# Kernel optimization log

Measured on AMD Instinct MI355X. Metric: run time of the kernel, lower is better.

## Reference

```python
import jax, jax.numpy as jnp
import numpy as np

# MLA dims (DeepSeek-V3-lite style)
B, S, DIM = 1, 2048, 2048
H, NOPE, ROPE, VD, LORA = 16, 128, 64, 128, 512
QK_HEAD = NOPE + ROPE  # 192
SCALE = QK_HEAD ** -0.5
EPS = 1e-6


def _rmsnorm(x, w):
    return x * jax.lax.rsqrt(jnp.mean(x * x, axis=-1, keepdims=True) + EPS) * w


def _apply_rope(x, cos, sin):
    # x: [b, s, h, d] with interleaved (real, imag) pairs; cos/sin: [s, d//2]
    x0, x1 = x[..., 0::2], x[..., 1::2]
    c = cos[None, :, None, :]
    s = sin[None, :, None, :]
    y0 = x0 * c - x1 * s
    y1 = x0 * s + x1 * c
    return jnp.stack([y0, y1], axis=-1).reshape(x.shape)


def setup_inputs() -> dict:
    key = jax.random.key(0)
    ks = jax.random.split(key, 6)
    x = jax.random.normal(ks[0], (B, S, DIM), jnp.float32) * 0.02
    wq = jax.random.normal(ks[1], (H * QK_HEAD, DIM), jnp.float32) * 0.02
    wkv_a = jax.random.normal(ks[2], (LORA + ROPE, DIM), jnp.float32) * 0.02
    kv_norm_w = jnp.ones((LORA,), jnp.float32)
    wkv_b = jax.random.normal(ks[3], (H * (NOPE + VD), LORA), jnp.float32) * 0.02
    wo = jax.random.normal(ks[4], (DIM, H * VD), jnp.float32) * 0.02
    # rotary freqs_cis (cos/sin) for qk_rope_head_dim
    inv_freq = 1.0 / (10000.0 ** (np.arange(0, ROPE, 2, dtype=np.float32) / ROPE))
    t = np.arange(S, dtype=np.float32)
    ang = np.outer(t, inv_freq)  # [S, ROPE//2]
    cos = jnp.asarray(np.cos(ang), jnp.float32)
    sin = jnp.asarray(np.sin(ang), jnp.float32)
    return {"x": x, "cos": cos, "sin": sin, "wq": wq, "wkv_a": wkv_a,
            "kv_norm_w": kv_norm_w, "wkv_b": wkv_b, "wo": wo}


def reference(x, cos, sin, wq, wkv_a, kv_norm_w, wkv_b, wo):
    b, s, _ = x.shape
    # queries
    q = (x @ wq.T).reshape(b, s, H, QK_HEAD)
    q_nope, q_pe = q[..., :NOPE], q[..., NOPE:]
    q_pe = _apply_rope(q_pe, cos, sin)  # [b,s,h,rope]
    # latent kv
    kv = x @ wkv_a.T  # [b,s,lora+rope]
    kv_c, k_pe = kv[..., :LORA], kv[..., LORA:]
    k_pe = _apply_rope(k_pe[:, :, None, :], cos, sin)[:, :, 0, :]  # [b,s,rope]
    kv_c = _rmsnorm(kv_c, kv_norm_w)  # latent kv cache [b,s,lora]
    # absorbed weights: wkv_b viewed as [h, nope+vd, lora]
    wkv_b_r = wkv_b.reshape(H, NOPE + VD, LORA)
    w_uk = wkv_b_r[:, :NOPE]   # [h, nope, lora]
    w_uv = wkv_b_r[:, NOPE:]   # [h, vd, lora]
    # absorb: project q_nope into latent space
    q_c = jnp.einsum('bshd,hdc->bshc', q_nope, w_uk)  # [b,s,h,lora]
    scores = (jnp.einsum('bshc,btc->bsht', q_c, kv_c)
              + jnp.einsum('bshr,btr->bsht', q_pe, k_pe)) * SCALE
    # causal mask over [s, t]
    mask = jnp.where(jnp.arange(s)[:, None] >= jnp.arange(s)[None, :], 0.0, -1e30)
    scores = scores + mask[None, :, None, :].astype(scores.dtype)
    attn = jax.nn.softmax(scores, axis=-1)
    o = jnp.einsum('bsht,btc->bshc', attn, kv_c)       # [b,s,h,lora]
    o = jnp.einsum('bshc,hdc->bshd', o, w_uv)           # [b,s,h,vd]
    out = o.reshape(b, s, H * VD) @ wo.T                # [b,s,dim]
    return out
```

## Files before the change

kernel.cpp:

```cpp
#include <hip/hip_runtime.h>
#include <hip/hip_bf16.h>
#include <math.h>

#define S_LEN 2048
#define DIM   2048
#define H_N   16
#define NOPE  128
#define ROPE  64
#define VD    128
#define LORA  512
#define D_QK  576
#define SCALE_F 0.07216878364870323f
#define EPS_F 1e-6f
#define KVF 640
#define KVS 1280

typedef short short8 __attribute__((ext_vector_type(8)));
typedef short short4v __attribute__((ext_vector_type(4)));
typedef float floatx4 __attribute__((ext_vector_type(4)));

static __device__ inline unsigned short f2bf_bits(float f) {
  union { __hip_bfloat16 h; unsigned short u; } cv;
  cv.h = __float2bfloat16(f);
  return cv.u;
}

static __device__ inline float bf2f(unsigned short b) {
  union { unsigned u; float f; } cv;
  cv.u = (unsigned)b << 16;
  return cv.f;
}

static __device__ inline void gload_lds16(const short* gptr, short* lds_base_uniform) {
  __builtin_amdgcn_global_load_lds(
      (const __attribute__((address_space(1))) void*)gptr,
      (__attribute__((address_space(3))) void*)lds_base_uniform, 16, 0, 0);
}

__global__ __launch_bounds__(256) void cast_f32_bf16(
    const float* __restrict__ src, short* __restrict__ dst, int n8) {
  int i = blockIdx.x * 256 + threadIdx.x;
  if (i < n8) {
    float4 a = ((const float4*)src)[2 * i];
    float4 b = ((const float4*)src)[2 * i + 1];
    uint4 o;
    o.x = (unsigned)f2bf_bits(a.x) | ((unsigned)f2bf_bits(a.y) << 16);
    o.y = (unsigned)f2bf_bits(a.z) | ((unsigned)f2bf_bits(a.w) << 16);
    o.z = (unsigned)f2bf_bits(b.x) | ((unsigned)f2bf_bits(b.y) << 16);
    o.w = (unsigned)f2bf_bits(b.z) | ((unsigned)f2bf_bits(b.w) << 16);
    ((uint4*)dst)[i] = o;
  }
}

__global__ __launch_bounds__(256) void zero_short8(short* __restrict__ dst, int n8) {
  int i = blockIdx.x * 256 + threadIdx.x;
  if (i < n8) ((uint4*)dst)[i] = (uint4){0u, 0u, 0u, 0u};
}

__global__ __launch_bounds__(256) void transpose_wuk(
    const float* __restrict__ wkvb, short* __restrict__ wukT) {
  __shared__ float tile[32][33];
  const int h = blockIdx.z, c0 = blockIdx.y * 32, d0 = blockIdx.x * 32;
  const int t = threadIdx.x;
  const int r = t >> 3, c4 = (t & 7) * 4;
  float4 v = *(const float4*)(wkvb + ((long)h * 256 + d0 + r) * 512 + c0 + c4);
  tile[r][c4 + 0] = v.x; tile[r][c4 + 1] = v.y;
  tile[r][c4 + 2] = v.z; tile[r][c4 + 3] = v.w;
  __syncthreads();
  uint2 o;
  o.x = (unsigned)f2bf_bits(tile[c4 + 0][r]) | ((unsigned)f2bf_bits(tile[c4 + 1][r]) << 16);
  o.y = (unsigned)f2bf_bits(tile[c4 + 2][r]) | ((unsigned)f2bf_bits(tile[c4 + 3][r]) << 16);
  *(uint2*)(wukT + ((long)h * 512 + c0 + r) * 128 + d0 + c4) = o;
}

__global__ __launch_bounds__(256) void gemm_bf16_nt(
    const short* __restrict__ A, const short* __restrict__ B, void* __restrict__ Cv,
    int K, int lda, int ldb, int ldc, long aB, long bB, long cB, int bf16out) {
  A += (long)blockIdx.z * aB;
  B += (long)blockIdx.z * bB;
  const int m0 = blockIdx.y * 128, n0 = blockIdx.x * 128;
  __shared__ short As[2][128 * 32];
  __shared__ short Bs[2][128 * 32];
  const int tid = threadIdx.x, w = tid >> 6, lane = tid & 63;
  const int ln = lane & 15, g = lane >> 4;
  const int mw = (w & 1) * 64, nw = (w >> 1) * 64;
  floatx4 acc[4][4];
#pragma unroll
  for (int i = 0; i < 4; ++i)
#pragma unroll
    for (int j = 0; j < 4; ++j) acc[i][j] = (floatx4){0.f, 0.f, 0.f, 0.f};

#define GEMM_STAGE(k0_, b_)                                                    \
  {                                                                            \
    _Pragma("unroll")                                                          \
    for (int i = 0; i < 2; ++i) {                                              \
      const int bc = (i * 4 + w) * 64;                                         \
      const int c = bc + lane;                                                 \
      const int row = c >> 2, quar = c & 3;                                    \
      gload_lds16(A + (long)(m0 + row) * lda + (k0_) + quar * 8, As[b_] + bc * 8); \
      gload_lds16(B + (long)(n0 + row) * ldb + (k0_) + quar * 8, Bs[b_] + bc * 8); \
    }                                                                          \
  }

  GEMM_STAGE(0, 0);
  __syncthreads();
  const int nk = K >> 5;
  for (int kt = 0; kt < nk; ++kt) {
    const int cb = kt & 1;
    if (kt + 1 < nk) GEMM_STAGE((kt + 1) << 5, cb ^ 1);
    short8 af[4], bf_[4];
#pragma unroll
    for (int mi = 0; mi < 4; ++mi)
      af[mi] = *(const short8*)(As[cb] + (mw + mi * 16 + ln) * 32 + g * 8);
#pragma unroll
    for (int ni = 0; ni < 4; ++ni)
      bf_[ni] = *(const short8*)(Bs[cb] + (nw + ni * 16 + ln) * 32 + g * 8);
#pragma unroll
    for (int mi = 0; mi < 4; ++mi)
#pragma unroll
      for (int ni = 0; ni < 4; ++ni)
        acc[mi][ni] = __builtin_amdgcn_mfma_f32_16x16x32_bf16(af[mi], bf_[ni], acc[mi][ni], 0, 0, 0);
    __syncthreads();
  }
#undef GEMM_STAGE
  if (bf16out) {
    short* Cs = (short*)Cv + (long)blockIdx.z * cB;
#pragma unroll
    for (int mi = 0; mi < 4; ++mi)
#pragma unroll
      for (int ni = 0; ni < 4; ++ni)
#pragma unroll
        for (int r = 0; r < 4; ++r)
          Cs[(long)(m0 + mw + mi * 16 + g * 4 + r) * ldc + n0 + nw + ni * 16 + ln] =
              (short)f2bf_bits(acc[mi][ni][r]);
  } else {
    float* C = (float*)Cv + (long)blockIdx.z * cB;
#pragma unroll
    for (int mi = 0; mi < 4; ++mi)
#pragma unroll
      for (int ni = 0; ni < 4; ++ni)
#pragma unroll
        for (int r = 0; r < 4; ++r)
          C[(long)(m0 + mw + mi * 16 + g * 4 + r) * ldc + n0 + nw + ni * 16 + ln] = acc[mi][ni][r];
  }
}

__global__ __launch_bounds__(64) void prep_kernel(
    float* kv, const short* __restrict__ qbufb, short* __restrict__ qhatb,
    const float* __restrict__ cosp, const float* __restrict__ sinp,
    const float* __restrict__ normw) {
  const int s = blockIdx.x;
  const int l = threadIdx.x;
  float* row = kv + (long)s * KVF;
  short* krow = (short*)kv + (long)s * KVS;

  float4 v0 = *(const float4*)(row + l * 8);
  float4 v1 = *(const float4*)(row + l * 8 + 4);
  float rx0 = 0.f, rx1 = 0.f, rc = 0.f, rs = 0.f;
  if (l < 32) {
    rc = cosp[s * 32 + l];
    rs = sinp[s * 32 + l];
    rx0 = row[512 + 2 * l];
    rx1 = row[512 + 2 * l + 1];
  }
  float4 w0 = *(const float4*)(normw + l * 8);
  float4 w1 = *(const float4*)(normw + l * 8 + 4);

  float ss = v0.x * v0.x + v0.y * v0.y + v0.z * v0.z + v0.w * v0.w +
             v1.x * v1.x + v1.y * v1.y + v1.z * v1.z + v1.w * v1.w;
#pragma unroll
  for (int off = 32; off; off >>= 1) ss += __shfl_xor(ss, off, 64);
  const float scale = rsqrtf(ss * (1.0f / (float)LORA) + EPS_F);
  v0.x *= scale * w0.x; v0.y *= scale * w0.y; v0.z *= scale * w0.z; v0.w *= scale * w0.w;
  v1.x *= scale * w1.x; v1.y *= scale * w1.y; v1.z *= scale * w1.z; v1.w *= scale * w1.w;

  uint4 pk;
  pk.x = (unsigned)f2bf_bits(v0.x) | ((unsigned)f2bf_bits(v0.y) << 16);
  pk.y = (unsigned)f2bf_bits(v0.z) | ((unsigned)f2bf_bits(v0.w) << 16);
  pk.z = (unsigned)f2bf_bits(v1.x) | ((unsigned)f2bf_bits(v1.y) << 16);
  pk.w = (unsigned)f2bf_bits(v1.z) | ((unsigned)f2bf_bits(v1.w) << 16);
  *(uint4*)(krow + l * 8) = pk;

  if (l < 32) {
    const float y0 = rx0 * rc - rx1 * rs;
    const float y1 = rx0 * rs + rx1 * rc;
    unsigned pr = (unsigned)f2bf_bits(y0) | ((unsigned)f2bf_bits(y1) << 16);
    *(unsigned*)(krow + 512 + 2 * l) = pr;
  }

#pragma unroll
  for (int it = 0; it < 8; ++it) {
    const int p = it * 64 + l;
    const int h = p >> 5;
    const int i = p & 31;
    const float c = cosp[s * 32 + i];
    const float sn = sinp[s * 32 + i];
    const short* qp = qbufb + (long)s * 3072 + h * 192 + NOPE;
    const unsigned uq = *(const unsigned*)(qp + 2 * i);
    const float x0 = bf2f((unsigned short)uq);
    const float x1 = bf2f((unsigned short)(uq >> 16));
    const float y0 = x0 * c - x1 * sn;
    const float y1 = x0 * sn + x1 * c;
    short* dst = qhatb + ((long)h * S_LEN + s) * D_QK + 512;
    *(unsigned*)(dst + 2 * i) = (unsigned)f2bf_bits(y0) | ((unsigned)f2bf_bits(y1) << 16);
  }
}

__global__ __launch_bounds__(256) void transpose_v(
    const short* __restrict__ kbf, short* __restrict__ kvt) {
  __shared__ short tile[32][36];
  const int d0 = blockIdx.x * 32;
  const int s0 = blockIdx.y * 32;
  const int t = threadIdx.x;
  const int r = t >> 3;
  const int c4 = (t & 7) * 4;
  uint2 v = *(const uint2*)(kbf + (long)(s0 + r) * KVS + d0 + c4);
  *(uint2*)(&tile[r][c4]) = v;
  __syncthreads();
  uint2 o;
  o.x = (unsigned)(unsigned short)tile[c4 + 0][r] | ((unsigned)(unsigned short)tile[c4 + 1][r] << 16);
  o.y = (unsigned)(unsigned short)tile[c4 + 2][r] | ((unsigned)(unsigned short)tile[c4 + 3][r] << 16);
  *(uint2*)(kvt + (long)(d0 + r) * S_LEN + s0 + c4) = o;
}

__global__ __launch_bounds__(256) void build_ktt(
    const short* __restrict__ kbf, short* __restrict__ ktt) {
  const int kt = blockIdx.x;
  for (int idx = threadIdx.x; idx < 18 * 64; idx += 256) {
    const int c = idx >> 6, l = idx & 63;
    const int ln = l & 15, g = l >> 4;
    uint4 v = *(const uint4*)(kbf + (long)(kt * 16 + ln) * KVS + c * 32 + g * 8);
    *(uint4*)(ktt + ((long)(kt * 18 + c) * 64 + l) * 8) = v;
  }
}

__global__ __launch_bounds__(256) void build_vtt(
    const short* __restrict__ kvt, short* __restrict__ vtt) {
  const int kt = blockIdx.x;
  for (int idx = threadIdx.x; idx < 32 * 64; idx += 256) {
    const int nt = idx >> 6, l = idx & 63;
    const int ln = l & 15, g = l >> 4;
    uint4 v = *(const uint4*)(kvt + (long)(nt * 16 + ln) * S_LEN + kt * 32 + g * 8);
    *(uint4*)(vtt + ((long)(kt * 32 + nt) * 64 + l) * 8) = v;
  }
}

__global__ __launch_bounds__(256, 2) void flash_reg(
    const short* __restrict__ qhat,
    const short* __restrict__ ktt,
    const short* __restrict__ vtt,
    short* __restrict__ obuf) {
  const int bid = blockIdx.x;
  const int hp = bid & 7;
  const int v = bid >> 3;
  const int vi = v & 31, vj = v >> 5;
  const int qw = (vj == 0) ? 127 - vi : (vj == 1) ? 64 + vi : (vj == 2) ? 63 - vi : vi;
  const int q0 = qw * 16;
  const int tid = threadIdx.x;
  const int w = tid >> 6;
  const int lane = tid & 63;
  const int ln = lane & 15, g = lane >> 4;
  const int h = hp * 2 + (w & 1);
  const int dh = w >> 1;
  const int vbase = dh * 256;
  const int qlim = q0 + ln;

  __shared__ short Kt[2][18 * 64 * 8];

  short8 qfr[18];
  {
    const short* qrow = qhat + ((long)h * S_LEN + q0 + ln) * D_QK;
#pragma unroll
    for (int c = 0; c < 18; ++c)
      qfr[c] = *(const short8*)(qrow + c * 32 + g * 8);
  }

  floatx4 oacc[16];
#pragma unroll
  for (int nt = 0; nt < 16; ++nt) oacc[nt] = (floatx4){0.f, 0.f, 0.f, 0.f};
  float lsum = 0.f;

  const int ntile = ((qw + 2) >> 1) * 2;

#define FL_STAGE(kt16_, b_)                                                    \
  {                                                                            \
    const short* ksrc_ = ktt + (long)(kt16_) * 18 * 512;                       \
    _Pragma("unroll")                                                          \
    for (int i = 0; i < 5; ++i) {                                              \
      const int grp = i * 4 + w;                                               \
      if (grp < 18)                                                            \
        gload_lds16(ksrc_ + (long)(grp * 64 + lane) * 8, Kt[b_] + grp * 512);  \
    }                                                                          \
  }

  FL_STAGE(0, 0);
  __syncthreads();

  floatx4 sA0, sA1, sB0, sB1;
  for (int t = 0; t < ntile; ++t) {
    const int cb = t & 1;
    if (t + 1 < ntile) FL_STAGE(t + 1, cb ^ 1);
    const short* kb = Kt[cb];
    floatx4 s0 = (floatx4){0.f, 0.f, 0.f, 0.f};
    floatx4 s1 = (floatx4){0.f, 0.f, 0.f, 0.f};
    __builtin_amdgcn_s_setprio(1);
#pragma unroll
    for (int c = 0; c < 18; c += 2) {
      short8 k0 = *(const short8*)(kb + (c * 64 + lane) * 8);
      short8 k1 = *(const short8*)(kb + ((c + 1) * 64 + lane) * 8);
      s0 = __builtin_amdgcn_mfma_f32_16x16x32_bf16(k0, qfr[c], s0, 0, 0, 0);
      s1 = __builtin_amdgcn_mfma_f32_16x16x32_bf16(k1, qfr[c + 1], s1, 0, 0, 0);
    }
    __builtin_amdgcn_s_setprio(0);
    if ((t & 1) == 0) {
      sA0 = s0; sA1 = s1;
    } else {
      sB0 = s0; sB1 = s1;
      const int p = t >> 1;
      const int t0 = p * 32;
      short4v pA4, pB4;
      float psum = 0.f;
#pragma unroll
      for (int r = 0; r < 4; ++r) {
        const int kAi = t0 + g * 4 + r;
        const int kBi = kAi + 16;
        float scA = fminf(fmaxf((sA0[r] + sA1[r]) * SCALE_F, -30.f), 30.f);
        float scB = fminf(fmaxf((sB0[r] + sB1[r]) * SCALE_F, -30.f), 30.f);
        float pA = (kAi <= qlim) ? __expf(scA) : 0.f;
        float pB = (kBi <= qlim) ? __expf(scB) : 0.f;
        psum += pA + pB;
        pA4[r] = (short)f2bf_bits(pA);
        pB4[r] = (short)f2bf_bits(pB);
      }
      lsum += psum;
      union { short4v s; int i[2]; } ua, ub;
      ua.s = pA4; ub.s = pB4;
      const int lolane = ln + ((g & 1) << 5);
      const int hilane = lolane + 16;
      int alo0 = __shfl(ua.i[0], lolane, 64), alo1 = __shfl(ua.i[1], lolane, 64);
      int ahi0 = __shfl(ua.i[0], hilane, 64), ahi1 = __shfl(ua.i[1], hilane, 64);
      int blo0 = __shfl(ub.i[0], lolane, 64), blo1 = __shfl(ub.i[1], lolane, 64);
      int bhi0 = __shfl(ub.i[0], hilane, 64), bhi1 = __shfl(ub.i[1], hilane, 64);
      union { short8 s; int i[4]; } up;
      const bool useA = (g < 2);
      up.i[0] = useA ? alo0 : blo0;
      up.i[1] = useA ? alo1 : blo1;
      up.i[2] = useA ? ahi0 : bhi0;
      up.i[3] = useA ? ahi1 : bhi1;
      const short8 pb8 = up.s;
      const short* vp = vtt + (((long)p * 32 + dh * 16) * 64 + lane) * 8;
#pragma unroll
      for (int half = 0; half < 2; ++half) {
        short8 va[8];
#pragma unroll
        for (int j = 0; j < 8; ++j)
          va[j] = *(const short8*)(vp + (half * 8 + j) * 512);
        __builtin_amdgcn_s_setprio(1);
#pragma unroll
        for (int j = 0; j < 8; ++j)
          oacc[half * 8 + j] = __builtin_amdgcn_mfma_f32_16x16x32_bf16(va[j], pb8, oacc[half * 8 + j], 0, 0, 0);
        __builtin_amdgcn_s_setprio(0);
      }
    }
    __syncthreads();
  }
#undef FL_STAGE

  lsum += __shfl_xor(lsum, 16, 64);
  lsum += __shfl_xor(lsum, 32, 64);
  const float inv = 1.0f / fmaxf(lsum, 1e-30f);

  short* orow = obuf + ((long)h * S_LEN + q0 + ln) * 512 + vbase + g * 4;
#pragma unroll
  for (int nt = 0; nt < 16; ++nt) {
    unsigned lo = (unsigned)f2bf_bits(oacc[nt][0] * inv) | ((unsigned)f2bf_bits(oacc[nt][1] * inv) << 16);
    unsigned hi = (unsigned)f2bf_bits(oacc[nt][2] * inv) | ((unsigned)f2bf_bits(oacc[nt][3] * inv) << 16);
    unsigned long long st = (unsigned long long)lo | ((unsigned long long)hi << 32);
    *(unsigned long long*)(orow + nt * 16) = st;
  }
}

extern "C" void kernel_launch(void* const* d_in, const int* in_sizes, int n_in,
                              void* d_out, int out_size, void* d_ws, size_t ws_size,
                              hipStream_t stream) {
  (void)in_sizes; (void)n_in; (void)out_size; (void)ws_size;
  const float* x      = (const float*)d_in[0];
  const float* cosp   = (const float*)d_in[1];
  const float* sinp   = (const float*)d_in[2];
  const float* wq     = (const float*)d_in[3];
  const float* wkv_a  = (const float*)d_in[4];
  const float* normw  = (const float*)d_in[5];
  const float* wkv_b  = (const float*)d_in[6];
  const float* wo     = (const float*)d_in[7];
  float* out = (float*)d_out;

  float* ws = (float*)d_ws;
  float* qbufR  = ws;
  float* kvold  = qbufR + (long)S_LEN * 3072;
  float* qhatR  = kvold + (long)S_LEN * D_QK;
  float* obufR  = qhatR + (long)H_N * S_LEN * D_QK;
  float* oprojR = obufR + (long)H_N * S_LEN * LORA;

  float* kvpad = oprojR;
  short* kbf = (short*)kvpad;
  short* wkvap = (short*)kvold;

  short* qbufb = (short*)qbufR;
  short* kvt = qbufb + (long)S_LEN * 3072;
  short* ktt = kvt + (long)512 * S_LEN;
  short* vtt = ktt + (long)128 * 18 * 64 * 8;

  short* qhatb  = (short*)qhatR;
  short* wkvbb  = qhatb + (long)H_N * S_LEN * D_QK;
  short* oprojb = wkvbb + (long)4096 * 512;
  short* wob    = oprojb + (long)2048 * 2048;

  short* xb   = (short*)obufR;
  short* wqb  = xb  + (long)2048 * 2048;
  short* wukT = wqb + (long)3072 * 2048;
  short* obufb = (short*)obufR;

  cast_f32_bf16<<<dim3(2048), 256, 0, stream>>>(x, xb, 2048 * 2048 / 8);
  cast_f32_bf16<<<dim3(3072), 256, 0, stream>>>(wq, wqb, 3072 * 2048 / 8);
  cast_f32_bf16<<<dim3(576), 256, 0, stream>>>(wkv_a, wkvap, 576 * 2048 / 8);
  zero_short8<<<dim3(64), 256, 0, stream>>>(wkvap + 576L * 2048, 64 * 2048 / 8);

  gemm_bf16_nt<<<dim3(3072 / 128, 2048 / 128, 1), 256, 0, stream>>>(
      xb, wqb, qbufb, 2048, 2048, 2048, 3072, 0, 0, 0, 1);

  gemm_bf16_nt<<<dim3(KVF / 128, 2048 / 128, 1), 256, 0, stream>>>(
      xb, wkvap, kvpad, 2048, 2048, 2048, KVF, 0, 0, 0, 0);

  prep_kernel<<<dim3(S_LEN), 64, 0, stream>>>(kvpad, qbufb, qhatb, cosp, sinp, normw);

  transpose_wuk<<<dim3(4, 16, 16), 256, 0, stream>>>(wkv_b, wukT);

  gemm_bf16_nt<<<dim3(512 / 128, 2048 / 128, 16), 256, 0, stream>>>(
      qbufb, wukT, qhatb, 128, 3072, 128, 576,
      192L, 512L * 128, (long)S_LEN * D_QK, 1);

  transpose_v<<<dim3(16, 64), 256, 0, stream>>>(kbf, kvt);
  build_ktt<<<dim3(128), 256, 0, stream>>>(kbf, ktt);
  build_vtt<<<dim3(64), 256, 0, stream>>>(kvt, vtt);

  flash_reg<<<dim3(1024), 256, 0, stream>>>(qhatb, ktt, vtt, obufb);

  cast_f32_bf16<<<dim3(1024), 256, 0, stream>>>(wkv_b, wkvbb, 4096 * 512 / 8);

  gemm_bf16_nt<<<dim3(1, 2048 / 128, 16), 256, 0, stream>>>(
      obufb, wkvbb + 128L * 512, oprojb, 512, 512, 512, 2048,
      (long)S_LEN * 512, 256L * 512, 128L, 1);

  cast_f32_bf16<<<dim3(2048), 256, 0, stream>>>(wo, wob, 2048 * 2048 / 8);
  gemm_bf16_nt<<<dim3(2048 / 128, 2048 / 128, 1), 256, 0, stream>>>(
      oprojb, wob, out, 2048, 2048, 2048, 2048, 0, 0, 0, 0);
}
```

Measured before the change: 468.8 us.

## Read K tiles directly from global memory instead of LDS double buffering

Removes the shared-memory double-buffered K staging and its per-tile block barriers from the attention kernel. Each wave now loads its K fragments straight from global memory (relying on L2/cache), computing both 16-key tiles of a pair in one iteration. This drops the LDS footprint and __syncthreads, so occupancy can rise and waves no longer stall on each other. The cost is redundant global/L2 traffic, since all four waves in a block re-read the same K data.

```diff
diff --git a/kernel.cpp b/kernel.cpp
--- a/kernel.cpp
+++ b/kernel.cpp
@@ -265,8 +265,6 @@
   const int vbase = dh * 256;
   const int qlim = q0 + ln;
 
-  __shared__ short Kt[2][18 * 64 * 8];
-
   short8 qfr[18];
   {
     const short* qrow = qhat + ((long)h * S_LEN + q0 + ln) * D_QK;
@@ -280,91 +278,73 @@
   for (int nt = 0; nt < 16; ++nt) oacc[nt] = (floatx4){0.f, 0.f, 0.f, 0.f};
   float lsum = 0.f;
 
-  const int ntile = ((qw + 2) >> 1) * 2;
-
-#define FL_STAGE(kt16_, b_)                                                    \
-  {                                                                            \
-    const short* ksrc_ = ktt + (long)(kt16_) * 18 * 512;                       \
-    _Pragma("unroll")                                                          \
-    for (int i = 0; i < 5; ++i) {                                              \
-      const int grp = i * 4 + w;                                               \
-      if (grp < 18)                                                            \
-        gload_lds16(ksrc_ + (long)(grp * 64 + lane) * 8, Kt[b_] + grp * 512);  \
-    }                                                                          \
-  }
-
-  FL_STAGE(0, 0);
-  __syncthreads();
-
-  floatx4 sA0, sA1, sB0, sB1;
-  for (int t = 0; t < ntile; ++t) {
-    const int cb = t & 1;
-    if (t + 1 < ntile) FL_STAGE(t + 1, cb ^ 1);
-    const short* kb = Kt[cb];
-    floatx4 s0 = (floatx4){0.f, 0.f, 0.f, 0.f};
-    floatx4 s1 = (floatx4){0.f, 0.f, 0.f, 0.f};
+  const int npairs = (qw + 2) >> 1;
+
+  for (int p = 0; p < npairs; ++p) {
+    const int t0 = p * 32;
+    const short* kbA = ktt + (long)(2 * p) * (18 * 512);
+    const short* kbB = kbA + 18 * 512;
+    floatx4 sA0 = (floatx4){0.f, 0.f, 0.f, 0.f};
+    floatx4 sA1 = (floatx4){0.f, 0.f, 0.f, 0.f};
+    floatx4 sB0 = (floatx4){0.f, 0.f, 0.f, 0.f};
+    floatx4 sB1 = (floatx4){0.f, 0.f, 0.f, 0.f};
     __builtin_amdgcn_s_setprio(1);
 #pragma unroll
     for (int c = 0; c < 18; c += 2) {
-      short8 k0 = *(const short8*)(kb + (c * 64 + lane) * 8);
-      short8 k1 = *(const short8*)(kb + ((c + 1) * 64 + lane) * 8);
-      s0 = __builtin_amdgcn_mfma_f32_16x16x32_bf16(k0, qfr[c], s0, 0, 0, 0);
-      s1 = __builtin_amdgcn_mfma_f32_16x16x32_bf16(k1, qfr[c + 1], s1, 0, 0, 0);
+      short8 a0 = *(const short8*)(kbA + (c * 64 + lane) * 8);
+      short8 a1 = *(const short8*)(kbA + ((c + 1) * 64 + lane) * 8);
+      short8 b0 = *(const short8*)(kbB + (c * 64 + lane) * 8);
+      short8 b1 = *(const short8*)(kbB + ((c + 1) * 64 + lane) * 8);
+      sA0 = __builtin_amdgcn_mfma_f32_16x16x32_bf16(a0, qfr[c], sA0, 0, 0, 0);
+      sB0 = __builtin_amdgcn_mfma_f32_16x16x32_bf16(b0, qfr[c], sB0, 0, 0, 0);
+      sA1 = __builtin_amdgcn_mfma_f32_16x16x32_bf16(a1, qfr[c + 1], sA1, 0, 0, 0);
+      sB1 = __builtin_amdgcn_mfma_f32_16x16x32_bf16(b1, qfr[c + 1], sB1, 0, 0, 0);
     }
     __builtin_amdgcn_s_setprio(0);
-    if ((t & 1) == 0) {
-      sA0 = s0; sA1 = s1;
-    } else {
-      sB0 = s0; sB1 = s1;
-      const int p = t >> 1;
-      const int t0 = p * 32;
-      short4v pA4, pB4;
-      float psum = 0.f;
-#pragma unroll
-      for (int r = 0; r < 4; ++r) {
-        const int kAi = t0 + g * 4 + r;
-        const int kBi = kAi + 16;
-        float scA = fminf(fmaxf((sA0[r] + sA1[r]) * SCALE_F, -30.f), 30.f);
-        float scB = fminf(fmaxf((sB0[r] + sB1[r]) * SCALE_F, -30.f), 30.f);
-        float pA = (kAi <= qlim) ? __expf(scA) : 0.f;
-        float pB = (kBi <= qlim) ? __expf(scB) : 0.f;
-        psum += pA + pB;
-        pA4[r] = (short)f2bf_bits(pA);
-        pB4[r] = (short)f2bf_bits(pB);
-      }
-      lsum += psum;
-      union { short4v s; int i[2]; } ua, ub;
-      ua.s = pA4; ub.s = pB4;
-      const int lolane = ln + ((g & 1) << 5);
-      const int hilane = lolane + 16;
-      int alo0 = __shfl(ua.i[0], lolane, 64), alo1 = __shfl(ua.i[1], lolane, 64);
-      int ahi0 = __shfl(ua.i[0], hilane, 64), ahi1 = __shfl(ua.i[1], hilane, 64);
-      int blo0 = __shfl(ub.i[0], lolane, 64), blo1 = __shfl(ub.i[1], lolane, 64);
-      int bhi0 = __shfl(ub.i[0], hilane, 64), bhi1 = __shfl(ub.i[1], hilane, 64);
-      union { short8 s; int i[4]; } up;
-      const bool useA = (g < 2);
-      up.i[0] = useA ? alo0 : blo0;
-      up.i[1] = useA ? alo1 : blo1;
-      up.i[2] = useA ? ahi0 : bhi0;
-      up.i[3] = useA ? ahi1 : bhi1;
-      const short8 pb8 = up.s;
-      const short* vp = vtt + (((long)p * 32 + dh * 16) * 64 + lane) * 8;
-#pragma unroll
-      for (int half = 0; half < 2; ++half) {
-        short8 va[8];
-#pragma unroll
-        for (int j = 0; j < 8; ++j)
-          va[j] = *(const short8*)(vp + (half * 8 + j) * 512);
-        __builtin_amdgcn_s_setprio(1);
-#pragma unroll
-        for (int j = 0; j < 8; ++j)
-          oacc[half * 8 + j] = __builtin_amdgcn_mfma_f32_16x16x32_bf16(va[j], pb8, oacc[half * 8 + j], 0, 0, 0);
-        __builtin_amdgcn_s_setprio(0);
-      }
+    short4v pA4, pB4;
+    float psum = 0.f;
+#pragma unroll
+    for (int r = 0; r < 4; ++r) {
+      const int kAi = t0 + g * 4 + r;
+      const int kBi = kAi + 16;
+      float scA = fminf(fmaxf((sA0[r] + sA1[r]) * SCALE_F, -30.f), 30.f);
+      float scB = fminf(fmaxf((sB0[r] + sB1[r]) * SCALE_F, -30.f), 30.f);
+      float pA = (kAi <= qlim) ? __expf(scA) : 0.f;
+      float pB = (kBi <= qlim) ? __expf(scB) : 0.f;
+      psum += pA + pB;
+      pA4[r] = (short)f2bf_bits(pA);
+      pB4[r] = (short)f2bf_bits(pB);
     }
-    __syncthreads();
-  }
-#undef FL_STAGE
+    lsum += psum;
+    union { short4v s; int i[2]; } ua, ub;
+    ua.s = pA4; ub.s = pB4;
+    const int lolane = ln + ((g & 1) << 5);
+    const int hilane = lolane + 16;
+    int alo0 = __shfl(ua.i[0], lolane, 64), alo1 = __shfl(ua.i[1], lolane, 64);
+    int ahi0 = __shfl(ua.i[0], hilane, 64), ahi1 = __shfl(ua.i[1], hilane, 64);
+    int blo0 = __shfl(ub.i[0], lolane, 64), blo1 = __shfl(ub.i[1], lolane, 64);
+    int bhi0 = __shfl(ub.i[0], hilane, 64), bhi1 = __shfl(ub.i[1], hilane, 64);
+    union { short8 s; int i[4]; } up;
+    const bool useA = (g < 2);
+    up.i[0] = useA ? alo0 : blo0;
+    up.i[1] = useA ? alo1 : blo1;
+    up.i[2] = useA ? ahi0 : bhi0;
+    up.i[3] = useA ? ahi1 : bhi1;
+    const short8 pb8 = up.s;
+    const short* vp = vtt + (((long)p * 32 + dh * 16) * 64 + lane) * 8;
+#pragma unroll
+    for (int half = 0; half < 2; ++half) {
+      short8 va[8];
+#pragma unroll
+      for (int j = 0; j < 8; ++j)
+        va[j] = *(const short8*)(vp + (half * 8 + j) * 512);
+      __builtin_amdgcn_s_setprio(1);
+#pragma unroll
+      for (int j = 0; j < 8; ++j)
+        oacc[half * 8 + j] = __builtin_amdgcn_mfma_f32_16x16x32_bf16(va[j], pb8, oacc[half * 8 + j], 0, 0, 0);
+      __builtin_amdgcn_s_setprio(0);
+    }
+  }
 
   lsum += __shfl_xor(lsum, 16, 64);
   lsum += __shfl_xor(lsum, 32, 64);
```

Measured after the change: 582.0 us. 24.1% more time.
